# Kernel optimization log

Hardware: AMD Instinct MI355X
Metric: run time of the kernel (lower is better)

The kernel has to match this reference:

```python
import jax, jax.numpy as jnp
import numpy as np

NUM_CLASSES = 16384
FEAT_DIM = 1024
ALPHA = 0.5


def setup_inputs() -> dict:
    key = jax.random.key(0)
    k1, k2, k3 = jax.random.split(key, 3)
    y_true = jax.random.randint(k1, (NUM_CLASSES,), 0, NUM_CLASSES, dtype=jnp.int32)
    y_pred = jax.random.normal(k2, (NUM_CLASSES, FEAT_DIM), dtype=jnp.float32)
    centers = jax.random.normal(k3, (NUM_CLASSES, FEAT_DIM), dtype=jnp.float32)
    return {"y_true": y_true, "y_pred": y_pred, "centers": centers}


def reference(y_true, y_pred, centers):
    # gather current centers per sample: [B, D]
    delta_centers = centers[y_true] - y_pred
    # per-class counts, gathered back per sample (tf.math.bincount semantics,
    # static length = NUM_CLASSES since all indices < NUM_CLASSES)
    counts = jnp.bincount(y_true, length=NUM_CLASSES)
    per_sample_counts = counts[y_true].astype(y_pred.dtype)  # [B]
    delta_centers = ALPHA * delta_centers / (per_sample_counts[:, None] + 1.0)
    # original code does an elementwise assign_sub (requires B == num_classes)
    new_centers = centers - delta_centers
    # MSE between features and the freshly-updated gathered centers
    diff = y_pred - new_centers[y_true]
    loss = jnp.mean(jnp.square(diff))
    return loss
```

## Files before the change

kernel.cpp:

```cpp
#include <hip/hip_runtime.h>

#define B 16384
#define D 1024
#define CL_ALPHA 0.5f
#define MAXM 16

__global__ void build_kernel(const int* __restrict__ y_true,
                             int* __restrict__ counts,
                             int* __restrict__ list) {
    int i = blockIdx.x * blockDim.x + threadIdx.x;
    if (i >= B) return;
    int j = y_true[i];
    int slot = atomicAdd(&counts[j], 1);
    if (slot < MAXM) list[j * MAXM + slot] = i;
}

__global__ __launch_bounds__(256) void class_kernel(const int* __restrict__ y_true,
                                                    const float* __restrict__ y_pred,
                                                    const float* __restrict__ centers,
                                                    const int* __restrict__ counts,
                                                    const int* __restrict__ list,
                                                    float* __restrict__ partials) {
    const int j = blockIdx.x;
    const int t = threadIdx.x;
    const int m = counts[j];
    if (m == 0) {
        if (t == 0) partials[j] = 0.0f;
        return;
    }

    __shared__ int mem[MAXM];
    if (t < MAXM) mem[t] = list[j * MAXM + t];

    const int kk = y_true[j];
    const float inv = CL_ALPHA / ((float)counts[kk] + 1.0f);

    float4 cj = ((const float4*)(centers + (size_t)j  * D))[t];
    float4 ck = ((const float4*)(centers + (size_t)kk * D))[t];
    float4 yj = ((const float4*)(y_pred  + (size_t)j  * D))[t];
    float4 corr;
    corr.x = inv * (ck.x - yj.x) - cj.x;
    corr.y = inv * (ck.y - yj.y) - cj.y;
    corr.z = inv * (ck.z - yj.z) - cj.z;
    corr.w = inv * (ck.w - yj.w) - cj.w;

    __syncthreads();

    float acc = 0.0f;
    const int mm = (m < MAXM) ? m : MAXM;
    for (int s = 0; s < mm; ++s) {
        const int i = mem[s];
        float4 a = ((const float4*)(y_pred + (size_t)i * D))[t];
        float dx = a.x + corr.x;
        float dy = a.y + corr.y;
        float dz = a.z + corr.z;
        float dw = a.w + corr.w;
        acc += dx * dx + dy * dy + dz * dz + dw * dw;
    }

    #pragma unroll
    for (int off = 32; off > 0; off >>= 1)
        acc += __shfl_down(acc, off, 64);

    __shared__ float smem[4];
    const int lane = t & 63;
    const int wave = t >> 6;
    if (lane == 0) smem[wave] = acc;
    __syncthreads();
    if (t == 0)
        partials[j] = smem[0] + smem[1] + smem[2] + smem[3];
}

__global__ __launch_bounds__(1024) void finalize_kernel(const float* __restrict__ partials,
                                                        float* __restrict__ out) {
    const int t = threadIdx.x;
    const float4* p4 = (const float4*)partials;
    float acc = 0.0f;
    #pragma unroll
    for (int w = 0; w < 4; ++w) {
        float4 v = p4[t + 1024 * w];
        acc += v.x + v.y + v.z + v.w;
    }
    #pragma unroll
    for (int off = 32; off > 0; off >>= 1)
        acc += __shfl_down(acc, off, 64);

    __shared__ float smem[16];
    const int lane = t & 63;
    const int wave = t >> 6;
    if (lane == 0) smem[wave] = acc;
    __syncthreads();
    if (t == 0) {
        float s = 0.0f;
        #pragma unroll
        for (int w = 0; w < 16; ++w) s += smem[w];
        out[0] = s * (1.0f / ((float)B * (float)D));
    }
}

extern "C" void kernel_launch(void* const* d_in, const int* in_sizes, int n_in,
                              void* d_out, int out_size, void* d_ws, size_t ws_size,
                              hipStream_t stream) {
    const int*   y_true  = (const int*)d_in[0];
    const float* y_pred  = (const float*)d_in[1];
    const float* centers = (const float*)d_in[2];
    float* out = (float*)d_out;

    int*   counts   = (int*)d_ws;
    float* partials = (float*)(counts + B);
    int*   list     = (int*)(partials + B);

    hipMemsetAsync(counts, 0, B * sizeof(int), stream);

    build_kernel<<<B / 256, 256, 0, stream>>>(y_true, counts, list);
    class_kernel<<<B, 256, 0, stream>>>(y_true, y_pred, centers, counts, list, partials);
    finalize_kernel<<<1, 1024, 0, stream>>>(partials, out);
}
```

Baseline: 158.5 us.

## Compact non-empty classes into a work list before the class kernel

Adds a prep kernel that atomically compacts classes with nonzero count into a metadata list holding class id, clamped member count, target center index and the precomputed scale factor. The class kernel now handles one compacted entry per block, so blocks beyond the work count exit immediately, and each block loads its member indices into registers instead of shared memory, which removes one barrier. The cost is an extra kernel launch, a larger memset that also zeroes the partials, and a global atomic counter. Roughly a third of the classes are empty, so about that many blocks become trivial exits.

```diff
diff --git a/kernel.cpp b/kernel.cpp
--- a/kernel.cpp
+++ b/kernel.cpp
@@ -15,25 +15,42 @@
     if (slot < MAXM) list[j * MAXM + slot] = i;
 }
 
-__global__ __launch_bounds__(256) void class_kernel(const int* __restrict__ y_true,
-                                                    const float* __restrict__ y_pred,
+__global__ void prep_kernel(const int* __restrict__ y_true,
+                            const int* __restrict__ counts,
+                            int* __restrict__ n_work,
+                            int4* __restrict__ meta) {
+    int j = blockIdx.x * blockDim.x + threadIdx.x;
+    if (j >= B) return;
+    int m = counts[j];
+    if (m == 0) return;
+    if (m > MAXM) m = MAXM;
+    int kk = y_true[j];
+    float inv = CL_ALPHA / ((float)counts[kk] + 1.0f);
+    int w = atomicAdd(n_work, 1);
+    meta[w] = make_int4(j | (m << 20), kk, __float_as_int(inv), 0);
+}
+
+__global__ __launch_bounds__(256) void class_kernel(const float* __restrict__ y_pred,
                                                     const float* __restrict__ centers,
-                                                    const int* __restrict__ counts,
+                                                    const int* __restrict__ n_work,
+                                                    const int4* __restrict__ meta,
                                                     const int* __restrict__ list,
                                                     float* __restrict__ partials) {
-    const int j = blockIdx.x;
+    const int nw = *n_work;
+    if ((int)blockIdx.x >= nw) return;
+
+    const int4 me = meta[blockIdx.x];
+    const int j  = me.x & 0xFFFFF;
+    const int mm = me.x >> 20;
+    const int kk = me.y;
+    const float inv = __int_as_float(me.z);
+
     const int t = threadIdx.x;
-    const int m = counts[j];
-    if (m == 0) {
-        if (t == 0) partials[j] = 0.0f;
-        return;
-    }
 
-    __shared__ int mem[MAXM];
-    if (t < MAXM) mem[t] = list[j * MAXM + t];
-
-    const int kk = y_true[j];
-    const float inv = CL_ALPHA / ((float)counts[kk] + 1.0f);
+    int idx[MAXM];
+    #pragma unroll
+    for (int s = 0; s < MAXM; ++s)
+        idx[s] = (s < mm) ? list[j * MAXM + s] : 0;
 
     float4 cj = ((const float4*)(centers + (size_t)j  * D))[t];
     float4 ck = ((const float4*)(centers + (size_t)kk * D))[t];
@@ -44,13 +61,9 @@
     corr.z = inv * (ck.z - yj.z) - cj.z;
     corr.w = inv * (ck.w - yj.w) - cj.w;
 
-    __syncthreads();
-
     float acc = 0.0f;
-    const int mm = (m < MAXM) ? m : MAXM;
     for (int s = 0; s < mm; ++s) {
-        const int i = mem[s];
-        float4 a = ((const float4*)(y_pred + (size_t)i * D))[t];
+        float4 a = ((const float4*)(y_pred + (size_t)idx[s] * D))[t];
         float dx = a.x + corr.x;
         float dy = a.y + corr.y;
         float dz = a.z + corr.z;
@@ -68,7 +81,7 @@
     if (lane == 0) smem[wave] = acc;
     __syncthreads();
     if (t == 0)
-        partials[j] = smem[0] + smem[1] + smem[2] + smem[3];
+        partials[blockIdx.x] = smem[0] + smem[1] + smem[2] + smem[3];
 }
 
 __global__ __launch_bounds__(1024) void finalize_kernel(const float* __restrict__ partials,
@@ -108,11 +121,14 @@
 
     int*   counts   = (int*)d_ws;
     float* partials = (float*)(counts + B);
-    int*   list     = (int*)(partials + B);
+    int*   n_work   = (int*)(partials + B);
+    int4*  meta     = (int4*)(n_work + 4);
+    int*   list     = (int*)(meta + B);
 
-    hipMemsetAsync(counts, 0, B * sizeof(int), stream);
+    hipMemsetAsync(d_ws, 0, (size_t)(2 * B + 4) * sizeof(int), stream);
 
     build_kernel<<<B / 256, 256, 0, stream>>>(y_true, counts, list);
-    class_kernel<<<B, 256, 0, stream>>>(y_true, y_pred, centers, counts, list, partials);
+    prep_kernel<<<B / 256, 256, 0, stream>>>(y_true, counts, n_work, meta);
+    class_kernel<<<B, 256, 0, stream>>>(y_pred, centers, n_work, meta, list, partials);
     finalize_kernel<<<1, 1024, 0, stream>>>(partials, out);
 }
```

Result: no change. 160.7 us (+1.3%).
